# Optimization experiments

Hardware: AMD Instinct MI355X
Metric: run time of the kernel (lower is better)

## Reference

```python
import jax, jax.numpy as jnp
from jax import lax
import numpy as np

FRAME_INTERVAL = 10  # module default


def _notaknot_slopes(yT):
    """First derivatives s_i of the not-a-knot cubic spline through yT.

    yT: (N, B) values at uniform integer knots t = 0..N-1 (h = 1).
    Matches scipy.interpolate.CubicSpline default bc_type='not-a-knot'.
    """
    n, B = yT.shape
    m = yT[1:] - yT[:-1]  # (N-1, B) secant slopes, h = 1
    # Tridiagonal system rows (scipy construction specialized to h = 1):
    #   row 0      :  1*s0 + 2*s1            = (5*m0 + m1)/2
    #   row i      :  s_{i-1} + 4*s_i + s_{i+1} = 3*(m_{i-1} + m_i)
    #   row n-1    :  2*s_{n-2} + 1*s_{n-1}  = (m_{n-3} + 5*m_{n-2})/2
    dt = yT.dtype
    lower = jnp.concatenate([jnp.zeros(1, dt), jnp.ones(n - 2, dt), jnp.full((1,), 2.0, dt)])
    main = jnp.concatenate([jnp.ones(1, dt), jnp.full((n - 2,), 4.0, dt), jnp.ones(1, dt)])
    upper = jnp.concatenate([jnp.full((1,), 2.0, dt), jnp.ones(n - 2, dt), jnp.zeros(1, dt)])
    rhs = jnp.concatenate([
        ((5.0 * m[0] + m[1]) / 2.0)[None],
        3.0 * (m[:-1] + m[1:]),
        ((m[-2] + 5.0 * m[-1]) / 2.0)[None],
    ])  # (N, B)

    # Thomas algorithm, batched over B via the carry.
    def fwd(carry, row):
        cp_prev, dp_prev = carry
        a, b, c, d = row
        denom = b - a * cp_prev
        cp = c / denom
        dp = (d - a * dp_prev) / denom
        return (cp, dp), (cp, dp)

    init = (jnp.zeros((), dt), jnp.zeros((B,), dt))
    _, (cp, dp) = lax.scan(fwd, init, (lower, main, upper, rhs))

    def bwd(x_next, row):
        cpi, dpi = row
        x = dpi - cpi * x_next
        return x, x

    _, s = lax.scan(bwd, jnp.zeros((B,), dt), (cp, dp), reverse=True)
    return s  # (N, B)


def _eval_spline(yT, s, sample_times):
    """Evaluate the cubic spline at integer sample_times. yT,s: (N,B)."""
    n = yT.shape[0]
    idx = jnp.clip(sample_times, 0, n - 2)
    t = (sample_times - idx).astype(yT.dtype)[:, None]  # local coord in [0,1]
    y0 = yT[idx]
    m = yT[idx + 1] - y0
    s0, s1 = s[idx], s[idx + 1]
    c2 = 3.0 * m - 2.0 * s0 - s1
    c3 = s0 + s1 - 2.0 * m
    return y0 + t * (s0 + t * (c2 + t * c3))  # (S, B)


def setup_inputs() -> dict:
    key = jax.random.key(0)
    k1, k2 = jax.random.split(key)
    B, N = 1024, 8192
    true_frames = jax.random.normal(k1, (B, N), dtype=jnp.float32)
    predicted_frames = jax.random.normal(k2, (B, N), dtype=jnp.float32)
    return {"true_frames": true_frames, "predicted_frames": predicted_frames}


def reference(true_frames, predicted_frames):
    B, N = true_frames.shape
    # Fit both splines in one batched solve: stack along batch -> (N, 2B).
    yT = jnp.concatenate([true_frames, predicted_frames], axis=0).T
    s = _notaknot_slopes(yT)
    sample_times = jnp.arange(0, N, FRAME_INTERVAL)
    vals = _eval_spline(yT, s, sample_times)  # (S, 2B)
    tv, pv = vals[:, :B], vals[:, B:]
    # per-sample mean over S then mean over batch == global mean
    return jnp.mean((tv - pv) ** 2)
```

## Files before the change

kernel.cpp:

```cpp
#include <hip/hip_runtime.h>
#include <hip/hip_bf16.h>


#define B_ROWS   1024
#define N_COLS   8192
#define STRIDE   10
#define N_SAMP   820
#define BLOCK    256

__global__ __launch_bounds__(BLOCK)
void spline_loss_kernel(const float* __restrict__ tf,
                        const float* __restrict__ pf,
                        float* __restrict__ out) {
    const int b = blockIdx.x;
    const float4* t4 = (const float4*)(tf + (size_t)b * N_COLS);
    const float4* p4 = (const float4*)(pf + (size_t)b * N_COLS);

    float acc = 0.0f;
    for (int g = threadIdx.x; g < N_COLS / 4; g += BLOCK) {
        float4 a = t4[g];
        float4 c = p4[g];
        int t = g << 2;
        float d0 = a.x - c.x;
        float d1 = a.y - c.y;
        float d2 = a.z - c.z;
        float d3 = a.w - c.w;
        if ((t    ) % STRIDE == 0) acc += d0 * d0;
        if ((t + 1) % STRIDE == 0) acc += d1 * d1;
        if ((t + 2) % STRIDE == 0) acc += d2 * d2;
        if ((t + 3) % STRIDE == 0) acc += d3 * d3;
    }

    #pragma unroll
    for (int off = 32; off > 0; off >>= 1)
        acc += __shfl_down(acc, off, 64);

    __shared__ float wsum[BLOCK / 64];
    const int lane = threadIdx.x & 63;
    const int wid  = threadIdx.x >> 6;
    if (lane == 0) wsum[wid] = acc;
    __syncthreads();

    if (threadIdx.x == 0) {
        float s = 0.0f;
        #pragma unroll
        for (int w = 0; w < BLOCK / 64; ++w) s += wsum[w];
        const float inv = 1.0f / (float)(B_ROWS * N_SAMP);
        atomicAdd(out, s * inv);
    }
}

extern "C" void kernel_launch(void* const* d_in, const int* in_sizes, int n_in,
                              void* d_out, int out_size, void* d_ws, size_t ws_size,
                              hipStream_t stream) {
    const float* tf = (const float*)d_in[0];
    const float* pf = (const float*)d_in[1];
    float* out = (float*)d_out;

    hipMemsetAsync(out, 0, sizeof(float), stream);

    spline_loss_kernel<<<B_ROWS, BLOCK, 0, stream>>>(tf, pf, out);
}
```

Measured before the change: 103.4 us.

## Split rows across two blocks, simplify sample mask, replace atomics with two-pass reduce

```diff
diff --git a/kernel.cpp b/kernel.cpp
--- a/kernel.cpp
+++ b/kernel.cpp
@@ -4,31 +4,33 @@
 
 #define B_ROWS   1024
 #define N_COLS   8192
-#define STRIDE   10
 #define N_SAMP   820
 #define BLOCK    256
+#define SPLIT    2
+#define GRID     (B_ROWS * SPLIT)
+#define GROUPS_PER_ROW   (N_COLS / 4)
+#define GROUPS_PER_BLOCK (GROUPS_PER_ROW / SPLIT)
 
 __global__ __launch_bounds__(BLOCK)
-void spline_loss_kernel(const float* __restrict__ tf,
-                        const float* __restrict__ pf,
-                        float* __restrict__ out) {
-    const int b = blockIdx.x;
+void spline_partial_kernel(const float* __restrict__ tf,
+                           const float* __restrict__ pf,
+                           float* __restrict__ partial) {
+    const int b    = blockIdx.x >> 1;
+    const int half = blockIdx.x & 1;
     const float4* t4 = (const float4*)(tf + (size_t)b * N_COLS);
     const float4* p4 = (const float4*)(pf + (size_t)b * N_COLS);
 
     float acc = 0.0f;
-    for (int g = threadIdx.x; g < N_COLS / 4; g += BLOCK) {
+    #pragma unroll
+    for (int k = 0; k < GROUPS_PER_BLOCK / BLOCK; ++k) {
+        const int g = half * GROUPS_PER_BLOCK + k * BLOCK + threadIdx.x;
         float4 a = t4[g];
         float4 c = p4[g];
-        int t = g << 2;
-        float d0 = a.x - c.x;
-        float d1 = a.y - c.y;
-        float d2 = a.z - c.z;
-        float d3 = a.w - c.w;
-        if ((t    ) % STRIDE == 0) acc += d0 * d0;
-        if ((t + 1) % STRIDE == 0) acc += d1 * d1;
-        if ((t + 2) % STRIDE == 0) acc += d2 * d2;
-        if ((t + 3) % STRIDE == 0) acc += d3 * d3;
+        const int r = g % 5;
+        const float d0 = a.x - c.x;
+        const float d2 = a.z - c.z;
+        acc += (r == 0) ? d0 * d0 : 0.0f;
+        acc += (r == 2) ? d2 * d2 : 0.0f;
     }
 
     #pragma unroll
@@ -45,8 +47,33 @@
         float s = 0.0f;
         #pragma unroll
         for (int w = 0; w < BLOCK / 64; ++w) s += wsum[w];
-        const float inv = 1.0f / (float)(B_ROWS * N_SAMP);
-        atomicAdd(out, s * inv);
+        partial[blockIdx.x] = s;
+    }
+}
+
+__global__ __launch_bounds__(BLOCK)
+void spline_final_kernel(const float* __restrict__ partial,
+                         float* __restrict__ out) {
+    float acc = 0.0f;
+    #pragma unroll
+    for (int k = 0; k < GRID / BLOCK; ++k)
+        acc += partial[k * BLOCK + threadIdx.x];
+
+    #pragma unroll
+    for (int off = 32; off > 0; off >>= 1)
+        acc += __shfl_down(acc, off, 64);
+
+    __shared__ float wsum[BLOCK / 64];
+    const int lane = threadIdx.x & 63;
+    const int wid  = threadIdx.x >> 6;
+    if (lane == 0) wsum[wid] = acc;
+    __syncthreads();
+
+    if (threadIdx.x == 0) {
+        float s = 0.0f;
+        #pragma unroll
+        for (int w = 0; w < BLOCK / 64; ++w) s += wsum[w];
+        out[0] = s * (1.0f / (float)(B_ROWS * N_SAMP));
     }
 }
 
@@ -55,9 +82,9 @@
                               hipStream_t stream) {
     const float* tf = (const float*)d_in[0];
     const float* pf = (const float*)d_in[1];
-    float* out = (float*)d_out;
+    float* out     = (float*)d_out;
+    float* partial = (float*)d_ws;
 
-    hipMemsetAsync(out, 0, sizeof(float), stream);
-
-    spline_loss_kernel<<<B_ROWS, BLOCK, 0, stream>>>(tf, pf, out);
+    spline_partial_kernel<<<GRID, BLOCK, 0, stream>>>(tf, pf, partial);
+    spline_final_kernel<<<1, BLOCK, 0, stream>>>(partial, out);
 }
```

New measurement: 93.30 us. 1.11x faster.
